# Kernel optimization log

Measured on AMD Instinct MI355X. Metric: run time of the kernel, lower is better.

Reference implementation:

```python
import jax, jax.numpy as jnp
import numpy as np


def setup_inputs() -> dict:
    key = jax.random.key(0)
    x = jax.random.normal(key, (4, 256, 64, 64), dtype=jnp.float32)
    return {"x": x}


def reference(x):
    b, c, h, w = x.shape
    n = h * w
    v = x.reshape(b, c, n)                     # [b, c, N]
    # energy[b, i, j] = sum_c x[b, c, i] * x[b, c, j]  (Q = K = V = flattened x)
    energy = jnp.einsum('bci,bcj->bij', v, v)  # [b, N, N]
    attn = jax.nn.softmax(energy, axis=-1)
    # out[b, c, i] = sum_j v[b, c, j] * attn[b, i, j]  (bmm(V, attn^T))
    out = jnp.einsum('bcj,bij->bci', v, attn)
    return out.reshape(b, c, h, w)
```

## Files before the change

kernel.cpp:

```cpp
#include <hip/hip_runtime.h>
#include <hip/hip_bf16.h>

typedef __bf16 bf16x8 __attribute__((ext_vector_type(8)));
typedef float f32x4 __attribute__((ext_vector_type(4)));

#define NB 4
#define NC 256
#define NN 4096
#define BK 32
#define NT 64

__device__ __forceinline__ void stage16(const void* g, void* l) {
    __builtin_amdgcn_global_load_lds(
        (const __attribute__((address_space(1))) unsigned int*)g,
        (__attribute__((address_space(3))) unsigned int*)l, 16, 0, 0);
}

__global__ __launch_bounds__(256) void prep_kernel(const float* __restrict__ x,
                                                   __bf16* __restrict__ xt,
                                                   __bf16* __restrict__ xv) {
    __shared__ __align__(16) __bf16 tile[64 * 64];
    const int b = blockIdx.z, c0 = blockIdx.y * 64, n0 = blockIdx.x * 64;
    const int t = threadIdx.x;
    {
        const int cc = t >> 2, nch = (t & 3) << 4;
        const float* src = x + ((size_t)(b * NC + c0 + cc)) * NN + n0 + nch;
        f32x4 v[4];
        v[0] = *(const f32x4*)(src);
        v[1] = *(const f32x4*)(src + 4);
        v[2] = *(const f32x4*)(src + 8);
        v[3] = *(const f32x4*)(src + 12);
        bf16x8 o[2];
#pragma unroll
        for (int q = 0; q < 2; ++q)
#pragma unroll
            for (int k = 0; k < 8; ++k)
                o[q][k] = (__bf16)v[q * 2 + (k >> 2)][k & 3];
        const int tile_idx = (n0 + nch) >> 5;
        const int off_j = nch & 31;
        __bf16* dstv = xv + (((size_t)(b * (NN / 32) + tile_idx)) * NC + (c0 + cc)) * 32 + off_j;
        *(bf16x8*)(dstv) = o[0];
        *(bf16x8*)(dstv + 8) = o[1];
        const int key = (cc ^ (cc >> 3)) & 7;
#pragma unroll
        for (int q = 0; q < 2; ++q) {
            int nc = (nch >> 3) + q;
            *(bf16x8*)(&tile[cc * 64 + ((nc ^ key) << 3)]) = o[q];
        }
    }
    __syncthreads();
    {
        const int nn = t >> 2, cch = (t & 3) << 4;
        bf16x8 o[2];
#pragma unroll
        for (int k = 0; k < 16; ++k) {
            int r = cch + k;
            int key = (r ^ (r >> 3)) & 7;
            o[k >> 3][k & 7] = tile[r * 64 + (((nn >> 3) ^ key) << 3) + (nn & 7)];
        }
        __bf16* dst = xt + ((size_t)(b * NN + n0 + nn)) * NC + c0 + cch;
        *(bf16x8*)(dst) = o[0];
        *(bf16x8*)(dst + 8) = o[1];
    }
}

__global__ __launch_bounds__(256, 2) void flash_kernel(const __bf16* __restrict__ xt,
                                                       const __bf16* __restrict__ xv,
                                                       float* __restrict__ out) {
    __shared__ __align__(16) __bf16 sK[2][2][BK * NC];
    __shared__ __align__(16) __bf16 sP[4][16 * BK];
    __shared__ float sML[4][16][2];

    const int bid = blockIdx.x;
    const int xcd = bid & 7;
    const int b = xcd >> 1;
    const int qblk = ((bid >> 3) << 1) | (xcd & 1);

    const int tid = threadIdx.x;
    const int w = tid >> 6;
    const int grp = w >> 1;
    const int wg = w & 1;
    const int lane = tid & 63;
    const int l16 = lane & 15;
    const int gq = lane >> 4;

    const int i_base = qblk * 32 + wg * 16;

    const char* xtb = (const char*)(xt + (size_t)b * NN * NC);
    const __bf16* vb0 = xv + (size_t)(b * (NN / 32)) * (NC * BK);

    bf16x8 qf[8];
    {
        const __bf16* qrow = (const __bf16*)xtb + (size_t)(i_base + l16) * NC + gq * 8;
#pragma unroll
        for (int ck = 0; ck < 8; ++ck) qf[ck] = *(const bf16x8*)(qrow + ck * 32);
    }

    f32x4 acc[16];
#pragma unroll
    for (int cf = 0; cf < 16; ++cf) acc[cf] = (f32x4){0.f, 0.f, 0.f, 0.f};
    float m_run[4], l_run[4];
#pragma unroll
    for (int r = 0; r < 4; ++r) { m_run[r] = -3.0e38f; l_run[r] = 0.f; }

    auto stage = [&](int bf, int t) {
        const int tj = grp * NT + t;
        const char* kb = xtb + (size_t)tj * BK * (NC * 2);
        __bf16* dk = &sK[grp][bf][0];
#pragma unroll
        for (int q = 0; q < 8; ++q) {
            int ci = wg * 8 + q;
            int rl = ci * 2 + (lane >> 5);
            int cs = (lane & 31) ^ (rl & 7);
            stage16(kb + rl * 512 + cs * 16, dk + ci * 512);
        }
    };

    stage(0, 0);
    __syncthreads();
    int cur = 0;

    for (int t = 0; t < NT; ++t) {
        const __bf16* vtile = vb0 + (size_t)(grp * NT + t) * (NC * BK);
        bf16x8 vv[16];
#pragma unroll
        for (int cf = 0; cf < 16; ++cf)
            vv[cf] = *(const bf16x8*)(vtile + (cf * 16 + l16) * BK + gq * 8);

        if (t + 1 < NT) stage(cur ^ 1, t + 1);

        const __bf16* kt = &sK[grp][cur][0];

        f32x4 s0 = (f32x4){0.f, 0.f, 0.f, 0.f};
        f32x4 s1 = (f32x4){0.f, 0.f, 0.f, 0.f};
#pragma unroll
        for (int ck = 0; ck < 8; ++ck) {
            int q = ck * 4 + gq;
            bf16x8 k0 = *(const bf16x8*)(kt + l16 * 256 + ((q ^ (l16 & 7)) << 3));
            s0 = __builtin_amdgcn_mfma_f32_16x16x32_bf16(qf[ck], k0, s0, 0, 0, 0);
            int row1 = 16 + l16;
            bf16x8 k1 = *(const bf16x8*)(kt + row1 * 256 + ((q ^ (row1 & 7)) << 3));
            s1 = __builtin_amdgcn_mfma_f32_16x16x32_bf16(qf[ck], k1, s1, 0, 0, 0);
        }

        float vmax[4];
#pragma unroll
        for (int r = 0; r < 4; ++r) {
            float v = fmaxf(s0[r], s1[r]);
            v = fmaxf(v, __shfl_xor(v, 1));
            v = fmaxf(v, __shfl_xor(v, 2));
            v = fmaxf(v, __shfl_xor(v, 4));
            v = fmaxf(v, __shfl_xor(v, 8));
            vmax[r] = v;
        }
        bool grow = (vmax[0] > m_run[0]) || (vmax[1] > m_run[1]) ||
                    (vmax[2] > m_run[2]) || (vmax[3] > m_run[3]);
        if (__any((int)grow)) {
#pragma unroll
            for (int r = 0; r < 4; ++r) {
                float nm = fmaxf(m_run[r], vmax[r]);
                float sc = __expf(m_run[r] - nm);
                m_run[r] = nm;
                l_run[r] *= sc;
#pragma unroll
                for (int cf = 0; cf < 16; ++cf) acc[cf][r] *= sc;
            }
        }
        float p0[4], p1[4];
#pragma unroll
        for (int r = 0; r < 4; ++r) {
            p0[r] = __expf(s0[r] - m_run[r]);
            p1[r] = __expf(s1[r] - m_run[r]);
            float v = p0[r] + p1[r];
            v += __shfl_xor(v, 1);
            v += __shfl_xor(v, 2);
            v += __shfl_xor(v, 4);
            v += __shfl_xor(v, 8);
            l_run[r] += v;
        }

        __bf16* myP = &sP[w][0];
#pragma unroll
        for (int r = 0; r < 4; ++r) {
            int i = gq * 4 + r;
            int key = (i >> 1) & 3;
            myP[i * 32 + (((l16 >> 3) ^ key) << 3) + (l16 & 7)] = (__bf16)p0[r];
            int j1 = 16 + l16;
            myP[i * 32 + (((j1 >> 3) ^ key) << 3) + (j1 & 7)] = (__bf16)p1[r];
        }
        bf16x8 pa = *(const bf16x8*)(&myP[l16 * 32 + ((gq ^ ((l16 >> 1) & 3)) << 3)]);

#pragma unroll
        for (int cf = 0; cf < 16; ++cf)
            acc[cf] = __builtin_amdgcn_mfma_f32_16x16x32_bf16(pa, vv[cf], acc[cf], 0, 0, 0);

        __syncthreads();
        cur ^= 1;
    }

    if (l16 == 0) {
#pragma unroll
        for (int r = 0; r < 4; ++r) {
            sML[w][gq * 4 + r][0] = m_run[r];
            sML[w][gq * 4 + r][1] = l_run[r];
        }
    }
    if (w >= 2) {
        float* F = ((float*)&sK[0][0][0]) + (size_t)(w - 2) * 4096;
#pragma unroll
        for (int cf = 0; cf < 16; ++cf)
#pragma unroll
            for (int r = 0; r < 4; ++r)
                F[cf * 256 + (gq * 4 + r) * 16 + l16] = acc[cf][r];
    }
    __syncthreads();
    if (w < 2) {
        const float* F = ((float*)&sK[0][0][0]) + (size_t)w * 4096;
        float sA[4], sB[4], inv[4];
#pragma unroll
        for (int r = 0; r < 4; ++r) {
            int i = gq * 4 + r;
            float mA = m_run[r], lA = l_run[r];
            float mB = sML[w + 2][i][0], lB = sML[w + 2][i][1];
            float m = fmaxf(mA, mB);
            float eA = __expf(mA - m), eB = __expf(mB - m);
            sA[r] = eA; sB[r] = eB;
            inv[r] = 1.f / (lA * eA + lB * eB);
        }
        float* sT = ((float*)&sP[0][0]) + (size_t)w * 288;
#pragma unroll
        for (int cf = 0; cf < 16; ++cf) {
#pragma unroll
            for (int r = 0; r < 4; ++r) {
                float o = (acc[cf][r] * sA[r] +
                           F[cf * 256 + (gq * 4 + r) * 16 + l16] * sB[r]) * inv[r];
                sT[(gq * 4 + r) * 17 + l16] = o;
            }
#pragma unroll
            for (int r = 0; r < 4; ++r) {
                int c = cf * 16 + gq + r * 4;
                out[((size_t)(b * NC + c)) * NN + i_base + l16] = sT[l16 * 17 + gq + r * 4];
            }
        }
    }
}

extern "C" void kernel_launch(void* const* d_in, const int* in_sizes, int n_in,
                              void* d_out, int out_size, void* d_ws, size_t ws_size,
                              hipStream_t stream) {
    const float* x = (const float*)d_in[0];
    float* out = (float*)d_out;
    __bf16* xt = (__bf16*)d_ws;
    __bf16* xv = xt + (size_t)NB * NN * NC;

    prep_kernel<<<dim3(NN / 64, NC / 64, NB), dim3(256), 0, stream>>>(x, xt, xv);
    flash_kernel<<<dim3(512), dim3(256), 0, stream>>>(xt, xv, out);
}
```

Measured before the change: 246.1 us.

## Rewrite flash loop with 32x32 MFMA, register-resident P, and four-way KV split

The attention kernel now uses 32x32x16 bf16 MFMA with a transposed S = K·Q^T, so P stays in registers. P is converted with v_cvt_pk_bf16_f32 and exchanged with v_permlane32_swap instead of going through LDS. Each of the four waves handles a quarter of the keys for all 32 queries, with Q staged once in LDS and K/V read straight from global memory. The three partial softmax states are merged at the end through LDS. This removes the per-tile LDS staging, the P round trip and the per-iteration block barriers, but it relies on cache hits for K/V global loads, uses many more registers for the 128-float accumulator, and adds a longer serial reduction epilogue.

```diff
diff --git a/kernel.cpp b/kernel.cpp
--- a/kernel.cpp
+++ b/kernel.cpp
@@ -3,17 +3,27 @@
 
 typedef __bf16 bf16x8 __attribute__((ext_vector_type(8)));
 typedef float f32x4 __attribute__((ext_vector_type(4)));
+typedef float f32x16 __attribute__((ext_vector_type(16)));
+typedef int int4v __attribute__((ext_vector_type(4)));
 
 #define NB 4
 #define NC 256
 #define NN 4096
 #define BK 32
-#define NT 64
+#define NT_W 32
 
 __device__ __forceinline__ void stage16(const void* g, void* l) {
     __builtin_amdgcn_global_load_lds(
         (const __attribute__((address_space(1))) unsigned int*)g,
         (__attribute__((address_space(3))) unsigned int*)l, 16, 0, 0);
+}
+__device__ __forceinline__ int cvtpk(float lo, float hi) {
+    int d;
+    asm("v_cvt_pk_bf16_f32 %0, %1, %2" : "=v"(d) : "v"(lo), "v"(hi));
+    return d;
+}
+__device__ __forceinline__ void plswap(int& a, int& b) {
+    asm("v_permlane32_swap_b32 %0, %1" : "+v"(a), "+v"(b));
 }
 
 __global__ __launch_bounds__(256) void prep_kernel(const float* __restrict__ x,
@@ -67,181 +77,152 @@
 __global__ __launch_bounds__(256, 2) void flash_kernel(const __bf16* __restrict__ xt,
                                                        const __bf16* __restrict__ xv,
                                                        float* __restrict__ out) {
-    __shared__ __align__(16) __bf16 sK[2][2][BK * NC];
-    __shared__ __align__(16) __bf16 sP[4][16 * BK];
-    __shared__ float sML[4][16][2];
+    __shared__ __align__(16) unsigned char smem[66560];
+    __bf16* sQ = (__bf16*)smem;
+    float* fb = (float*)smem;
+    float* sML = (float*)(smem + 65536);
 
     const int bid = blockIdx.x;
     const int xcd = bid & 7;
     const int b = xcd >> 1;
     const int qblk = ((bid >> 3) << 1) | (xcd & 1);
+    const int i_base = qblk * 32;
 
     const int tid = threadIdx.x;
     const int w = tid >> 6;
-    const int grp = w >> 1;
-    const int wg = w & 1;
     const int lane = tid & 63;
-    const int l16 = lane & 15;
-    const int gq = lane >> 4;
-
-    const int i_base = qblk * 32 + wg * 16;
-
-    const char* xtb = (const char*)(xt + (size_t)b * NN * NC);
-    const __bf16* vb0 = xv + (size_t)(b * (NN / 32)) * (NC * BK);
-
-    bf16x8 qf[8];
-    {
-        const __bf16* qrow = (const __bf16*)xtb + (size_t)(i_base + l16) * NC + gq * 8;
-#pragma unroll
-        for (int ck = 0; ck < 8; ++ck) qf[ck] = *(const bf16x8*)(qrow + ck * 32);
-    }
-
-    f32x4 acc[16];
-#pragma unroll
-    for (int cf = 0; cf < 16; ++cf) acc[cf] = (f32x4){0.f, 0.f, 0.f, 0.f};
-    float m_run[4], l_run[4];
-#pragma unroll
-    for (int r = 0; r < 4; ++r) { m_run[r] = -3.0e38f; l_run[r] = 0.f; }
-
-    auto stage = [&](int bf, int t) {
-        const int tj = grp * NT + t;
-        const char* kb = xtb + (size_t)tj * BK * (NC * 2);
-        __bf16* dk = &sK[grp][bf][0];
-#pragma unroll
-        for (int q = 0; q < 8; ++q) {
-            int ci = wg * 8 + q;
-            int rl = ci * 2 + (lane >> 5);
-            int cs = (lane & 31) ^ (rl & 7);
-            stage16(kb + rl * 512 + cs * 16, dk + ci * 512);
-        }
-    };
-
-    stage(0, 0);
-    __syncthreads();
-    int cur = 0;
-
-    for (int t = 0; t < NT; ++t) {
-        const __bf16* vtile = vb0 + (size_t)(grp * NT + t) * (NC * BK);
-        bf16x8 vv[16];
-#pragma unroll
-        for (int cf = 0; cf < 16; ++cf)
-            vv[cf] = *(const bf16x8*)(vtile + (cf * 16 + l16) * BK + gq * 8);
-
-        if (t + 1 < NT) stage(cur ^ 1, t + 1);
-
-        const __bf16* kt = &sK[grp][cur][0];
-
-        f32x4 s0 = (f32x4){0.f, 0.f, 0.f, 0.f};
-        f32x4 s1 = (f32x4){0.f, 0.f, 0.f, 0.f};
-#pragma unroll
-        for (int ck = 0; ck < 8; ++ck) {
-            int q = ck * 4 + gq;
-            bf16x8 k0 = *(const bf16x8*)(kt + l16 * 256 + ((q ^ (l16 & 7)) << 3));
-            s0 = __builtin_amdgcn_mfma_f32_16x16x32_bf16(qf[ck], k0, s0, 0, 0, 0);
-            int row1 = 16 + l16;
-            bf16x8 k1 = *(const bf16x8*)(kt + row1 * 256 + ((q ^ (row1 & 7)) << 3));
-            s1 = __builtin_amdgcn_mfma_f32_16x16x32_bf16(qf[ck], k1, s1, 0, 0, 0);
-        }
-
-        float vmax[4];
-#pragma unroll
-        for (int r = 0; r < 4; ++r) {
-            float v = fmaxf(s0[r], s1[r]);
-            v = fmaxf(v, __shfl_xor(v, 1));
-            v = fmaxf(v, __shfl_xor(v, 2));
-            v = fmaxf(v, __shfl_xor(v, 4));
-            v = fmaxf(v, __shfl_xor(v, 8));
-            vmax[r] = v;
-        }
-        bool grow = (vmax[0] > m_run[0]) || (vmax[1] > m_run[1]) ||
-                    (vmax[2] > m_run[2]) || (vmax[3] > m_run[3]);
-        if (__any((int)grow)) {
-#pragma unroll
-            for (int r = 0; r < 4; ++r) {
-                float nm = fmaxf(m_run[r], vmax[r]);
-                float sc = __expf(m_run[r] - nm);
-                m_run[r] = nm;
-                l_run[r] *= sc;
-#pragma unroll
-                for (int cf = 0; cf < 16; ++cf) acc[cf][r] *= sc;
+    const int li = lane & 31;
+    const int hi = lane >> 5;
+
+    const __bf16* xtb = xt + (size_t)b * NN * NC;
+
+#pragma unroll
+    for (int r4 = 0; r4 < 4; ++r4) {
+        int d = r4 * 256 + w * 64 + lane;
+        int row = d >> 5;
+        int u = (d & 31) ^ (row & 31);
+        stage16(xtb + (size_t)(i_base + row) * NC + u * 8, sQ + (size_t)(r4 * 256 + w * 64) * 8);
+    }
+    __syncthreads();
+
+    f32x16 acc[8];
+#pragma unroll
+    for (int ch = 0; ch < 8; ++ch) acc[ch] = (f32x16)0.f;
+    float m_run = -3.0e38f, l_part = 0.f;
+
+    const __bf16* kRow = xtb + (size_t)(w * 1024) * NC + li * NC + hi * 8;
+    const __bf16* vRow = xv + ((size_t)(b * 128 + w * 32)) * (NC * BK) + li * BK + hi * 8;
+
+    for (int t = 0; t < NT_W; ++t) {
+        f32x16 s = (f32x16)0.f;
+#pragma unroll
+        for (int cstep = 0; cstep < 16; ++cstep) {
+            bf16x8 kf = *(const bf16x8*)(kRow + cstep * 16);
+            bf16x8 qf = *(const bf16x8*)(sQ + li * 256 + ((((cstep << 1) | hi) ^ li) << 3));
+            s = __builtin_amdgcn_mfma_f32_32x32x16_bf16(kf, qf, s, 0, 0, 0);
+        }
+
+        float t0 = fmaxf(fmaxf(s[0], s[1]), fmaxf(s[2], s[3]));
+        float t1 = fmaxf(fmaxf(s[4], s[5]), fmaxf(s[6], s[7]));
+        float t2 = fmaxf(fmaxf(s[8], s[9]), fmaxf(s[10], s[11]));
+        float t3 = fmaxf(fmaxf(s[12], s[13]), fmaxf(s[14], s[15]));
+        float tmax = fmaxf(fmaxf(t0, t1), fmaxf(t2, t3));
+        if (__any((int)(tmax > m_run))) {
+            float om = __shfl_xor(tmax, 32);
+            float nm = fmaxf(m_run, fmaxf(tmax, om));
+            float sc = __expf(m_run - nm);
+            m_run = nm;
+            l_part *= sc;
+#pragma unroll
+            for (int ch = 0; ch < 8; ++ch)
+#pragma unroll
+                for (int r = 0; r < 16; ++r) acc[ch][r] *= sc;
+        }
+        float p[16];
+#pragma unroll
+        for (int r = 0; r < 16; ++r) p[r] = __expf(s[r] - m_run);
+        l_part += (((p[0] + p[1]) + (p[2] + p[3])) + ((p[4] + p[5]) + (p[6] + p[7]))) +
+                  (((p[8] + p[9]) + (p[10] + p[11])) + ((p[12] + p[13]) + (p[14] + p[15])));
+
+        int a0 = cvtpk(p[0], p[1]),   b0 = cvtpk(p[4], p[5]);
+        int a1 = cvtpk(p[2], p[3]),   b1 = cvtpk(p[6], p[7]);
+        int a2 = cvtpk(p[8], p[9]),   b2 = cvtpk(p[12], p[13]);
+        int a3 = cvtpk(p[10], p[11]), b3 = cvtpk(p[14], p[15]);
+        plswap(a0, b0);
+        plswap(a1, b1);
+        plswap(a2, b2);
+        plswap(a3, b3);
+        bf16x8 B0 = __builtin_bit_cast(bf16x8, (int4v){a0, a1, b0, b1});
+        bf16x8 B1 = __builtin_bit_cast(bf16x8, (int4v){a2, a3, b2, b3});
+
+#pragma unroll
+        for (int ch = 0; ch < 8; ++ch) {
+            const __bf16* vp = vRow + ch * 1024;
+            bf16x8 v0 = *(const bf16x8*)(vp);
+            bf16x8 v1 = *(const bf16x8*)(vp + 16);
+            acc[ch] = __builtin_amdgcn_mfma_f32_32x32x16_bf16(v0, B0, acc[ch], 0, 0, 0);
+            acc[ch] = __builtin_amdgcn_mfma_f32_32x32x16_bf16(v1, B1, acc[ch], 0, 0, 0);
+        }
+
+        kRow += BK * NC;
+        vRow += NC * BK;
+    }
+
+    float l_full = l_part + __shfl_xor(l_part, 32);
+    if (lane < 32) {
+        sML[(w * 32 + li) * 2 + 0] = m_run;
+        sML[(w * 32 + li) * 2 + 1] = l_full;
+    }
+    __syncthreads();
+    float mw[4], lw[4];
+#pragma unroll
+    for (int k = 0; k < 4; ++k) {
+        mw[k] = sML[(k * 32 + li) * 2 + 0];
+        lw[k] = sML[(k * 32 + li) * 2 + 1];
+    }
+    float ms = fmaxf(fmaxf(mw[0], mw[1]), fmaxf(mw[2], mw[3]));
+    float lsum = 0.f;
+#pragma unroll
+    for (int k = 0; k < 4; ++k) lsum += lw[k] * __expf(mw[k] - ms);
+    const float inv = 1.f / lsum;
+    const float f_own = __expf(m_run - ms);
+#pragma unroll
+    for (int ch = 0; ch < 8; ++ch)
+#pragma unroll
+        for (int r = 0; r < 16; ++r) acc[ch][r] *= f_own;
+
+    if (w >= 2) {
+        float* dst = fb + (size_t)(w - 2) * 8192;
+#pragma unroll
+        for (int ch = 0; ch < 8; ++ch)
+#pragma unroll
+            for (int r = 0; r < 16; ++r) dst[(ch * 16 + r) * 64 + lane] = acc[ch][r];
+    }
+    __syncthreads();
+    if (w < 2) {
+        const float* srcf = fb + (size_t)w * 8192;
+#pragma unroll
+        for (int ch = 0; ch < 8; ++ch)
+#pragma unroll
+            for (int r = 0; r < 16; ++r) acc[ch][r] += srcf[(ch * 16 + r) * 64 + lane];
+    }
+    __syncthreads();
+    if (w == 1) {
+#pragma unroll
+        for (int ch = 0; ch < 8; ++ch)
+#pragma unroll
+            for (int r = 0; r < 16; ++r) fb[(ch * 16 + r) * 64 + lane] = acc[ch][r];
+    }
+    __syncthreads();
+    if (w == 0) {
+#pragma unroll
+        for (int ch = 0; ch < 8; ++ch)
+#pragma unroll
+            for (int r = 0; r < 16; ++r) {
+                float o = (acc[ch][r] + fb[(ch * 16 + r) * 64 + lane]) * inv;
+                int c = ch * 32 + (r & 3) + ((r >> 2) << 3) + (hi << 2);
+                out[((size_t)(b * NC + c)) * NN + i_base + li] = o;
             }
-        }
-        float p0[4], p1[4];
-#pragma unroll
-        for (int r = 0; r < 4; ++r) {
-            p0[r] = __expf(s0[r] - m_run[r]);
-            p1[r] = __expf(s1[r] - m_run[r]);
-            float v = p0[r] + p1[r];
-            v += __shfl_xor(v, 1);
-            v += __shfl_xor(v, 2);
-            v += __shfl_xor(v, 4);
-            v += __shfl_xor(v, 8);
-            l_run[r] += v;
-        }
-
-        __bf16* myP = &sP[w][0];
-#pragma unroll
-        for (int r = 0; r < 4; ++r) {
-            int i = gq * 4 + r;
-            int key = (i >> 1) & 3;
-            myP[i * 32 + (((l16 >> 3) ^ key) << 3) + (l16 & 7)] = (__bf16)p0[r];
-            int j1 = 16 + l16;
-            myP[i * 32 + (((j1 >> 3) ^ key) << 3) + (j1 & 7)] = (__bf16)p1[r];
-        }
-        bf16x8 pa = *(const bf16x8*)(&myP[l16 * 32 + ((gq ^ ((l16 >> 1) & 3)) << 3)]);
-
-#pragma unroll
-        for (int cf = 0; cf < 16; ++cf)
-            acc[cf] = __builtin_amdgcn_mfma_f32_16x16x32_bf16(pa, vv[cf], acc[cf], 0, 0, 0);
-
-        __syncthreads();
-        cur ^= 1;
-    }
-
-    if (l16 == 0) {
-#pragma unroll
-        for (int r = 0; r < 4; ++r) {
-            sML[w][gq * 4 + r][0] = m_run[r];
-            sML[w][gq * 4 + r][1] = l_run[r];
-        }
-    }
-    if (w >= 2) {
-        float* F = ((float*)&sK[0][0][0]) + (size_t)(w - 2) * 4096;
-#pragma unroll
-        for (int cf = 0; cf < 16; ++cf)
-#pragma unroll
-            for (int r = 0; r < 4; ++r)
-                F[cf * 256 + (gq * 4 + r) * 16 + l16] = acc[cf][r];
-    }
-    __syncthreads();
-    if (w < 2) {
-        const float* F = ((float*)&sK[0][0][0]) + (size_t)w * 4096;
-        float sA[4], sB[4], inv[4];
-#pragma unroll
-        for (int r = 0; r < 4; ++r) {
-            int i = gq * 4 + r;
-            float mA = m_run[r], lA = l_run[r];
-            float mB = sML[w + 2][i][0], lB = sML[w + 2][i][1];
-            float m = fmaxf(mA, mB);
-            float eA = __expf(mA - m), eB = __expf(mB - m);
-            sA[r] = eA; sB[r] = eB;
-            inv[r] = 1.f / (lA * eA + lB * eB);
-        }
-        float* sT = ((float*)&sP[0][0]) + (size_t)w * 288;
-#pragma unroll
-        for (int cf = 0; cf < 16; ++cf) {
-#pragma unroll
-            for (int r = 0; r < 4; ++r) {
-                float o = (acc[cf][r] * sA[r] +
-                           F[cf * 256 + (gq * 4 + r) * 16 + l16] * sB[r]) * inv[r];
-                sT[(gq * 4 + r) * 17 + l16] = o;
-            }
-#pragma unroll
-            for (int r = 0; r < 4; ++r) {
-                int c = cf * 16 + gq + r * 4;
-                out[((size_t)(b * NC + c)) * NN + i_base + l16] = sT[l16 * 17 + gq + r * 4];
-            }
-        }
     }
 }
 
```

Measured after the change: 256.3 us. 4.1% more time.
